# Optimization experiments

Hardware: AMD Instinct MI355X
Metric: run time of the kernel (lower is better)

Reference implementation:

```python
import jax, jax.numpy as jnp
import numpy as np

WL_W = 8   # weight quantization bits (args.wl_weight)
WL_A = 8   # activation quantization bits (args.wl_activate)
EPS = 1e-5


def _quant_ste(x, bits):
    """Symmetric per-tensor uniform quantization with straight-through estimator,
    emulating NeuroSim's wage-style weight/activation quantization in QConv2d."""
    n = float(2 ** (bits - 1) - 1)
    s = jnp.max(jnp.abs(x)) + 1e-12
    xq = jnp.round(x / s * n) / n * s
    return x + jax.lax.stop_gradient(xq - x)


def _qconv(x, w):
    # quantize input and weight, then 3x3 conv, stride 1, padding 1 (NCHW/OIHW)
    xq = _quant_ste(x, WL_A)
    wq = _quant_ste(w, WL_W)
    return jax.lax.conv_general_dilated(
        xq, wq, window_strides=(1, 1), padding=((1, 1), (1, 1)),
        dimension_numbers=('NCHW', 'OIHW', 'NCHW'))


def _bn(x, gamma, beta):
    # training-mode BatchNorm2d: batch statistics over (N, H, W)
    mean = jnp.mean(x, axis=(0, 2, 3), keepdims=True)
    var = jnp.var(x, axis=(0, 2, 3), keepdims=True)
    xn = (x - mean) * jax.lax.rsqrt(var + EPS)
    return xn * gamma[None, :, None, None] + beta[None, :, None, None]


def setup_inputs() -> dict:
    key = jax.random.key(0)
    ks = jax.random.split(key, 3)
    B, C, H, W = 32, 128, 56, 56
    return {
        'x': jax.random.normal(ks[0], (B, C, H, W), dtype=jnp.float32),
        'w1': jax.random.normal(ks[1], (C, C, 3, 3), dtype=jnp.float32) * 0.05,
        'gamma1': jnp.ones((C,), dtype=jnp.float32),
        'beta1': jnp.zeros((C,), dtype=jnp.float32),
        'w2': jax.random.normal(ks[2], (C, C, 3, 3), dtype=jnp.float32) * 0.05,
        'gamma2': jnp.ones((C,), dtype=jnp.float32),
        'beta2': jnp.zeros((C,), dtype=jnp.float32),
    }


def reference(x, w1, gamma1, beta1, w2, gamma2, beta2):
    identity = x  # no downsample
    out = _qconv(x, w1)
    out = _bn(out, gamma1, beta1)
    out = jax.nn.relu(out)
    out = _qconv(out, w2)
    out = _bn(out, gamma2, beta2)
    out = out + identity
    return jax.nn.relu(out)
```

## Files before the change

### kernel.cpp

```cpp
#include <hip/hip_runtime.h>

#define NB 32
#define C 128
#define H 56
#define W 56
#define HWSZ (H*W)
#define ELTS (NB*C*HWSZ)
#define NHW (NB*HWSZ)
#define HP 59
#define SLAB 8192
#define GCONVX 28
#define NBLK (GCONVX*NB)
#define NBLK2 (NBLK*2)
#define PSTRIDE2 (C*NBLK2)

typedef __attribute__((ext_vector_type(8))) short bf16x8;
typedef __attribute__((ext_vector_type(4))) short short4v;
typedef __attribute__((ext_vector_type(4))) float f32x4;
typedef __attribute__((ext_vector_type(4))) int i32x4;

#define SLOT_SX 0
#define SLOT_SW1 1
#define SLOT_SW2 2
#define SLOT_SA2 3
#define SCALE1 8
#define SHIFT1 136
#define SCALE2 264
#define SHIFT2 392

#define META_OFF 0ull
#define META_BYTES 8192ull
#define XQ_OFF 8192ull
#define XQ_BYTES ((unsigned long long)NB*HP*SLAB)
#define A2Q_OFF (XQ_OFF + XQ_BYTES)
#define Y1_OFF (A2Q_OFF + XQ_BYTES)
#define Y_BYTES ((unsigned long long)ELTS*2ull)
#define Y2_OFF (Y1_OFF + Y_BYTES)
#define W1Q_OFF (Y2_OFF + Y_BYTES)
#define WQ_BYTES (9ull*2*128*64)
#define W2Q_OFF (W1Q_OFF + WQ_BYTES)
#define PART_OFF (W2Q_OFF + WQ_BYTES)
#define PART_BYTES (4ull*PSTRIDE2*4ull)

__device__ __forceinline__ short f2bf_rne(float f) {
    unsigned u = __float_as_uint(f);
    return (short)((u + 0x7FFFu + ((u >> 16) & 1u)) >> 16);
}
__device__ __forceinline__ float bf2f(short s) {
    return __uint_as_float(((unsigned)(unsigned short)s) << 16);
}

__global__ void absmax_kernel(const float* __restrict__ p, int n4, unsigned* __restrict__ slot) {
    __shared__ float red[256];
    float m = 0.f;
    int stride = gridDim.x * blockDim.x;
    for (int i = blockIdx.x * blockDim.x + threadIdx.x; i < n4; i += stride) {
        f32x4 v = ((const f32x4*)p)[i];
        m = fmaxf(m, fmaxf(fmaxf(fabsf(v.x), fabsf(v.y)), fmaxf(fabsf(v.z), fabsf(v.w))));
    }
    red[threadIdx.x] = m;
    __syncthreads();
    for (int s = 128; s > 0; s >>= 1) {
        if (threadIdx.x < s) red[threadIdx.x] = fmaxf(red[threadIdx.x], red[threadIdx.x + s]);
        __syncthreads();
    }
    if (threadIdx.x == 0) atomicMax(slot, __float_as_uint(red[0]));
}

__global__ void absmax_w_kernel(const float* __restrict__ w1, const float* __restrict__ w2,
                                unsigned* __restrict__ metau) {
    __shared__ float red[256];
    const float* p = blockIdx.y ? w2 : w1;
    unsigned* slot = metau + (blockIdx.y ? SLOT_SW2 : SLOT_SW1);
    const int n4 = 147456 / 4;
    float m = 0.f;
    int stride = gridDim.x * blockDim.x;
    for (int i = blockIdx.x * blockDim.x + threadIdx.x; i < n4; i += stride) {
        f32x4 v = ((const f32x4*)p)[i];
        m = fmaxf(m, fmaxf(fmaxf(fabsf(v.x), fabsf(v.y)), fmaxf(fabsf(v.z), fabsf(v.w))));
    }
    red[threadIdx.x] = m;
    __syncthreads();
    for (int s = 128; s > 0; s >>= 1) {
        if (threadIdx.x < s) red[threadIdx.x] = fmaxf(red[threadIdx.x], red[threadIdx.x + s]);
        __syncthreads();
    }
    if (threadIdx.x == 0) atomicMax(slot, __float_as_uint(red[0]));
}

__global__ void pad_zero_kernel(char* __restrict__ xq, char* __restrict__ a2q,
                                float* __restrict__ meta) {
    int hp = blockIdx.x;
    int n = blockIdx.y;
    char* base = (blockIdx.z ? a2q : xq) + ((size_t)n * HP + hp) * SLAB;
    int t = threadIdx.x;
    if (blockIdx.z == 0 && blockIdx.x == 0 && blockIdx.y == 0) {
        #pragma unroll
        for (int j = 0; j < 8; ++j) meta[j * 256 + t] = 0.f;
    }
    if (hp == 0 || hp >= 57) {
        f32x4 z = {0.f, 0.f, 0.f, 0.f};
        *(f32x4*)(base + t * 16) = z;
        *(f32x4*)(base + 4096 + t * 16) = z;
    } else {
        if (t < 32) *(int*)(base + t * 4) = 0;
        else        *(int*)(base + 7296 + (t - 32) * 4) = 0;
    }
}

__global__ void quant_w_kernel(const float* __restrict__ w1, const float* __restrict__ w2,
                               const float* __restrict__ meta,
                               char* __restrict__ w1q, char* __restrict__ w2q) {
    const float* w = blockIdx.y ? w2 : w1;
    char* wq = blockIdx.y ? w2q : w1q;
    float qs = 127.f / (meta[blockIdx.y ? SLOT_SW2 : SLOT_SW1] + 1e-12f);
    int idx = blockIdx.x * 256 + threadIdx.x;
    int co = idx >> 7, ci = idx & 127;
    const float* src = w + ((size_t)(co * 128 + ci)) * 9;
    int cc = ci >> 6, cl = ci & 63;
    #pragma unroll
    for (int tap = 0; tap < 9; ++tap) {
        int q = (int)rintf(src[tap] * qs);
        wq[(((size_t)tap * 2 + cc) * 128 + co) * 64 + cl] = (char)q;
    }
}

__global__ void quant_x_kernel(const float* __restrict__ x, const float* __restrict__ meta,
                               char* __restrict__ xq) {
    __shared__ float tile[128][57];
    int h = blockIdx.x, n = blockIdx.y, t = threadIdx.x;
    int ci = t >> 1, seg = (t & 1) * 28;
    const float* row = x + (((size_t)(n * C + ci)) * H + h) * W + seg;
    #pragma unroll
    for (int j = 0; j < 28; j += 4) {
        f32x4 v = *(const f32x4*)(row + j);
        tile[ci][seg + j + 0] = v.x;
        tile[ci][seg + j + 1] = v.y;
        tile[ci][seg + j + 2] = v.z;
        tile[ci][seg + j + 3] = v.w;
    }
    __syncthreads();
    float qs = 127.f / (meta[SLOT_SX] + 1e-12f);
    int w = t & 63, cq = t >> 6;
    if (w < 56) {
        char* slab = xq + ((size_t)n * HP + (h + 1)) * SLAB;
        int wp = w + 1;
        #pragma unroll
        for (int c2 = 0; c2 < 2; ++c2) {
            union { char c[16]; i32x4 v; } u;
            #pragma unroll
            for (int j = 0; j < 16; ++j)
                u.c[j] = (char)(int)rintf(tile[cq * 32 + c2 * 16 + j][w] * qs);
            int L = wp * 128 + cq * 32 + c2 * 16;
            *(i32x4*)(slab + (L ^ ((wp & 7) << 4))) = u.v;
        }
    }
}

__global__ __launch_bounds__(256, 4) void conv_mfma_kernel(
        const char* __restrict__ xq, const char* __restrict__ wq,
        short* __restrict__ y, const float* __restrict__ meta,
        float* __restrict__ part, int slot_in, int slot_w) {
    __shared__ __align__(16) char lds[4 * SLAB + 512];
    const int n = blockIdx.y, h0 = blockIdx.x * 2;
    const int t = threadIdx.x, lane = t & 63;
    const int wv = t >> 6, r = wv >> 1, ch = (wv & 1) * 64;
    const int l15 = lane & 15, lg = lane >> 4;

    const char* slabbase = xq + ((size_t)n * HP + h0) * SLAB;
    #pragma unroll
    for (int s = 0; s < 4; ++s) {
        #pragma unroll
        for (int i = 0; i < 2; ++i) {
            int off = (i * 256 + t) * 16;
            __builtin_amdgcn_global_load_lds(
                (const __attribute__((address_space(1))) unsigned*)(slabbase + s * SLAB + off),
                (__attribute__((address_space(3))) unsigned*)(lds + s * SLAB + off), 16, 0, 0);
        }
    }

    i32x4 acc[4][4] = {};

    #pragma unroll
    for (int kh = 0; kh < 3; ++kh) {
        if (kh == 0)      { asm volatile("s_waitcnt vmcnt(4)" ::: "memory"); }
        else if (kh == 1) { asm volatile("s_waitcnt vmcnt(2)" ::: "memory"); }
        else              { asm volatile("s_waitcnt vmcnt(0)" ::: "memory"); }
        __builtin_amdgcn_s_barrier();
        const char* Bb = lds + (kh + r) * SLAB;
        #pragma unroll
        for (int kw = 0; kw < 3; ++kw) {
            #pragma unroll
            for (int cc = 0; cc < 2; ++cc) {
                const char* wt = wq + (((kh * 3 + kw) * 2 + cc) << 13);
                i32x4 a[4];
                #pragma unroll
                for (int ct = 0; ct < 4; ++ct)
                    a[ct] = *(const i32x4*)(wt + (ch + ct * 16 + l15) * 64 + lg * 16);
                #pragma unroll
                for (int fj = 0; fj < 4; ++fj) {
                    int wpp = fj * 16 + l15 + kw;
                    int L = (wpp << 7) + (cc << 6) + (lg << 4);
                    i32x4 b = *(const i32x4*)(Bb + (L ^ ((wpp & 7) << 4)));
                    #pragma unroll
                    for (int ct = 0; ct < 4; ++ct)
                        acc[ct][fj] = __builtin_amdgcn_mfma_i32_16x16x64_i8(a[ct], b, acc[ct][fj], 0, 0, 0);
                }
            }
        }
    }

    float dq = (meta[slot_in] + 1e-12f) * (meta[slot_w] + 1e-12f) * (1.f / 16129.f);
    short* yrow = y + (((size_t)n * H + (h0 + r)) * W) * C;
    int bcol = (blockIdx.y * GCONVX + blockIdx.x) * 2 + r;

    #pragma unroll
    for (int ct = 0; ct < 4; ++ct) {
        float s1[4] = {}, s2[4] = {}, m1[4], m2[4];
        #pragma unroll
        for (int q = 0; q < 4; ++q) { m1[q] = -1e30f; m2[q] = -1e30f; }
        #pragma unroll
        for (int fj = 0; fj < 4; ++fj) {
            int wo = fj * 16 + l15;
            if (wo < W) {
                short4v pk;
                #pragma unroll
                for (int q = 0; q < 4; ++q) {
                    float v = (float)acc[ct][fj][q] * dq;
                    s1[q] += v;
                    s2[q] += v * v;
                    m1[q] = fmaxf(m1[q], v);
                    m2[q] = fmaxf(m2[q], -v);
                    pk[q] = f2bf_rne(v);
                }
                *(short4v*)(yrow + (size_t)wo * C + ch + ct * 16 + lg * 4) = pk;
            }
        }
        #pragma unroll
        for (int q = 0; q < 4; ++q) {
            #pragma unroll
            for (int m = 1; m < 16; m <<= 1) {
                s1[q] += __shfl_xor(s1[q], m, 64);
                s2[q] += __shfl_xor(s2[q], m, 64);
                m1[q] = fmaxf(m1[q], __shfl_xor(m1[q], m, 64));
                m2[q] = fmaxf(m2[q], __shfl_xor(m2[q], m, 64));
            }
        }
        if (l15 == 0) {
            #pragma unroll
            for (int q = 0; q < 4; ++q) {
                int cch = ch + ct * 16 + lg * 4 + q;
                part[0 * PSTRIDE2 + (size_t)cch * NBLK2 + bcol] = s1[q];
                part[1 * PSTRIDE2 + (size_t)cch * NBLK2 + bcol] = s2[q];
                part[2 * PSTRIDE2 + (size_t)cch * NBLK2 + bcol] = m1[q];
                part[3 * PSTRIDE2 + (size_t)cch * NBLK2 + bcol] = m2[q];
            }
        }
    }
}

__global__ void bn_reduce_kernel(const float* __restrict__ part, float* __restrict__ meta,
                                 const float* __restrict__ gamma, const float* __restrict__ beta,
                                 int scale_off, int shift_off, int amax_slot) {
    __shared__ float r1[256], r2[256], r3[256], r4[256];
    int c = blockIdx.x, t = threadIdx.x;
    const float* ps = part + 0 * PSTRIDE2 + (size_t)c * NBLK2;
    const float* pq = part + 1 * PSTRIDE2 + (size_t)c * NBLK2;
    const float* pm = part + 2 * PSTRIDE2 + (size_t)c * NBLK2;
    const float* pn = part + 3 * PSTRIDE2 + (size_t)c * NBLK2;
    float s1 = 0.f, s2 = 0.f, m1 = -1e30f, m2 = -1e30f;
    for (int i = t; i < NBLK2; i += 256) {
        s1 += ps[i];
        s2 += pq[i];
        m1 = fmaxf(m1, pm[i]);
        m2 = fmaxf(m2, pn[i]);
    }
    r1[t] = s1; r2[t] = s2; r3[t] = m1; r4[t] = m2;
    __syncthreads();
    for (int k = 128; k > 0; k >>= 1) {
        if (t < k) {
            r1[t] += r1[t + k];
            r2[t] += r2[t + k];
            r3[t] = fmaxf(r3[t], r3[t + k]);
            r4[t] = fmaxf(r4[t], r4[t + k]);
        }
        __syncthreads();
    }
    if (t == 0) {
        float mean = r1[0] * (1.f / NHW);
        float var = r2[0] * (1.f / NHW) - mean * mean;
        float istd = rsqrtf(var + 1e-5f);
        float sc = gamma[c] * istd;
        float sh = beta[c] - mean * sc;
        meta[scale_off + c] = sc;
        meta[shift_off + c] = sh;
        if (amax_slot >= 0) {
            float cand = fmaxf(0.f, fmaxf(sc * r3[0] + sh, sc * (-r4[0]) + sh));
            atomicMax((unsigned*)meta + amax_slot, __float_as_uint(cand));
        }
    }
}

__global__ void quant_bnrelu_kernel(const short* __restrict__ y1, const float* __restrict__ meta,
                                    char* __restrict__ a2q) {
    int h = blockIdx.x, n = blockIdx.y, t = threadIdx.x;
    const short* row = y1 + (((size_t)n * H + h) * W) * C;
    float qs = 127.f / (meta[SLOT_SA2] + 1e-12f);
    char* slab = a2q + ((size_t)n * HP + (h + 1)) * SLAB;
    #pragma unroll
    for (int i = 0; i < 2; ++i) {
        int g = i * 256 + t;
        if (g < 448) {
            int w = g >> 3, cg = g & 7;
            bf16x8 v0 = *(const bf16x8*)(row + w * 128 + cg * 16);
            bf16x8 v1 = *(const bf16x8*)(row + w * 128 + cg * 16 + 8);
            union { char c[16]; i32x4 v; } u;
            #pragma unroll
            for (int j = 0; j < 8; ++j) {
                float a = fmaxf(bf2f(v0[j]) * meta[SCALE1 + cg * 16 + j] + meta[SHIFT1 + cg * 16 + j], 0.f);
                u.c[j] = (char)(int)rintf(a * qs);
            }
            #pragma unroll
            for (int j = 0; j < 8; ++j) {
                float a = fmaxf(bf2f(v1[j]) * meta[SCALE1 + cg * 16 + 8 + j] + meta[SHIFT1 + cg * 16 + 8 + j], 0.f);
                u.c[8 + j] = (char)(int)rintf(a * qs);
            }
            int wp = w + 1;
            int L = wp * 128 + cg * 16;
            *(i32x4*)(slab + (L ^ ((wp & 7) << 4))) = u.v;
        }
    }
}

__global__ void final_kernel(const short* __restrict__ y2, const float* __restrict__ x,
                             const float* __restrict__ meta, float* __restrict__ out) {
    __shared__ short tile[56 * 128];
    int h = blockIdx.x, n = blockIdx.y, t = threadIdx.x;
    const short* row = y2 + (((size_t)n * H + h) * W) * C;
    #pragma unroll
    for (int i = 0; i < 4; ++i) {
        int g = i * 256 + t;
        if (g < 896) *(bf16x8*)(tile + g * 8) = *(const bf16x8*)(row + g * 8);
    }
    __syncthreads();
    int c = t >> 1, seg = (t & 1) * 28;
    float sc = meta[SCALE2 + c], sh = meta[SHIFT2 + c];
    const float* xr = x + (((size_t)(n * C + c)) * H + h) * W + seg;
    float* orow = out + (((size_t)(n * C + c)) * H + h) * W + seg;
    #pragma unroll
    for (int j = 0; j < 28; j += 4) {
        f32x4 xv = *(const f32x4*)(xr + j);
        f32x4 o;
        #pragma unroll
        for (int k = 0; k < 4; ++k) {
            float yv = bf2f(tile[(seg + j + k) * 128 + c]);
            o[k] = fmaxf(yv * sc + sh + xv[k], 0.f);
        }
        *(f32x4*)(orow + j) = o;
    }
}

extern "C" void kernel_launch(void* const* d_in, const int* in_sizes, int n_in,
                              void* d_out, int out_size, void* d_ws, size_t ws_size,
                              hipStream_t stream) {
    const float* x      = (const float*)d_in[0];
    const float* w1     = (const float*)d_in[1];
    const float* gamma1 = (const float*)d_in[2];
    const float* beta1  = (const float*)d_in[3];
    const float* w2     = (const float*)d_in[4];
    const float* gamma2 = (const float*)d_in[5];
    const float* beta2  = (const float*)d_in[6];
    float* out = (float*)d_out;
    char* ws = (char*)d_ws;

    float* meta = (float*)(ws + META_OFF);
    unsigned* metau = (unsigned*)meta;
    char* xq   = ws + XQ_OFF;
    char* a2q  = ws + A2Q_OFF;
    short* y1  = (short*)(ws + Y1_OFF);
    short* y2  = (short*)(ws + Y2_OFF);
    char* w1q  = ws + W1Q_OFF;
    char* w2q  = ws + W2Q_OFF;
    float* part = (float*)(ws + PART_OFF);

    pad_zero_kernel<<<dim3(59, 32, 2), 256, 0, stream>>>(xq, a2q, meta);

    absmax_kernel<<<1024, 256, 0, stream>>>(x, ELTS / 4, metau + SLOT_SX);
    absmax_w_kernel<<<dim3(64, 2), 256, 0, stream>>>(w1, w2, metau);
    quant_w_kernel<<<dim3(64, 2), 256, 0, stream>>>(w1, w2, meta, w1q, w2q);

    dim3 ghn(56, 32);
    quant_x_kernel<<<ghn, 256, 0, stream>>>(x, meta, xq);

    dim3 gconv(GCONVX, 32);
    conv_mfma_kernel<<<gconv, 256, 0, stream>>>(xq, w1q, y1, meta, part, SLOT_SX, SLOT_SW1);
    bn_reduce_kernel<<<128, 256, 0, stream>>>(part, meta, gamma1, beta1, SCALE1, SHIFT1, SLOT_SA2);
    quant_bnrelu_kernel<<<ghn, 256, 0, stream>>>(y1, meta, a2q);

    conv_mfma_kernel<<<gconv, 256, 0, stream>>>(a2q, w2q, y2, meta, part, SLOT_SA2, SLOT_SW2);
    bn_reduce_kernel<<<128, 256, 0, stream>>>(part, meta, gamma2, beta2, SCALE2, SHIFT2, -1);

    final_kernel<<<ghn, 256, 0, stream>>>(y2, x, meta, out);
}
```

Baseline: 266.0 us.

## Stage conv output through LDS and restructure BN partial-stat reduction layout

The conv epilogue now writes bf16 results into swizzled LDS and then stores full rows to global memory with 16-byte coalesced writes, instead of scattered 8-byte writes. Per-block BN partial statistics are staged in LDS and written contiguously per block. The BN reduction is split into a 64-block kernel that reduces with atomicAdd and order-preserving atomicMax into meta, plus a small finalize kernel. The aim is to cut uncoalesced global traffic and strided partial reads, at the cost of an extra launch and extra LDS use. It also relies on the meta accumulators being zeroed beforehand, which the shown pad_zero/meta setup must guarantee.

Result: slower. 278.1 us (+4.5%).

```diff
diff --git a/kernel.cpp b/kernel.cpp
--- a/kernel.cpp
+++ b/kernel.cpp
@@ -12,7 +12,6 @@
 #define GCONVX 28
 #define NBLK (GCONVX*NB)
 #define NBLK2 (NBLK*2)
-#define PSTRIDE2 (C*NBLK2)
 
 typedef __attribute__((ext_vector_type(8))) short bf16x8;
 typedef __attribute__((ext_vector_type(4))) short short4v;
@@ -23,10 +22,18 @@
 #define SLOT_SW1 1
 #define SLOT_SW2 2
 #define SLOT_SA2 3
-#define SCALE1 8
-#define SHIFT1 136
-#define SCALE2 264
-#define SHIFT2 392
+#define SUM1 8
+#define SSQ1 136
+#define MAXE1 264
+#define MAXNEG1 392
+#define SCALE1 520
+#define SHIFT1 648
+#define SUM2 776
+#define SSQ2 904
+#define MAXE2 1032
+#define MAXNEG2 1160
+#define SCALE2 1288
+#define SHIFT2 1416
 
 #define META_OFF 0ull
 #define META_BYTES 8192ull
@@ -40,7 +47,7 @@
 #define WQ_BYTES (9ull*2*128*64)
 #define W2Q_OFF (W1Q_OFF + WQ_BYTES)
 #define PART_OFF (W2Q_OFF + WQ_BYTES)
-#define PART_BYTES (4ull*PSTRIDE2*4ull)
+#define PART_BYTES ((unsigned long long)NBLK2*512*4)
 
 __device__ __forceinline__ short f2bf_rne(float f) {
     unsigned u = __float_as_uint(f);
@@ -48,6 +55,14 @@
 }
 __device__ __forceinline__ float bf2f(short s) {
     return __uint_as_float(((unsigned)(unsigned short)s) << 16);
+}
+__device__ __forceinline__ unsigned fenc(float f) {
+    unsigned u = __float_as_uint(f);
+    return (u & 0x80000000u) ? ~u : (u | 0x80000000u);
+}
+__device__ __forceinline__ float fdec(unsigned e) {
+    unsigned u = (e & 0x80000000u) ? (e ^ 0x80000000u) : ~e;
+    return __uint_as_float(u);
 }
 
 __global__ void absmax_kernel(const float* __restrict__ p, int n4, unsigned* __restrict__ slot) {
@@ -211,8 +226,10 @@
     }
 
     float dq = (meta[slot_in] + 1e-12f) * (meta[slot_w] + 1e-12f) * (1.f / 16129.f);
-    short* yrow = y + (((size_t)n * H + (h0 + r)) * W) * C;
-    int bcol = (blockIdx.y * GCONVX + blockIdx.x) * 2 + r;
+
+    __syncthreads();
+    char* ylds = lds;
+    float* slds = (float*)(lds + 28672);
 
     #pragma unroll
     for (int ct = 0; ct < 4; ++ct) {
@@ -233,7 +250,8 @@
                     m2[q] = fmaxf(m2[q], -v);
                     pk[q] = f2bf_rne(v);
                 }
-                *(short4v*)(yrow + (size_t)wo * C + ch + ct * 16 + lg * 4) = pk;
+                int a = r * 14336 + wo * 256 + ch * 2 + ct * 32 + lg * 8;
+                *(short4v*)(ylds + (a ^ ((wo & 7) << 4))) = pk;
             }
         }
         #pragma unroll
@@ -249,55 +267,82 @@
         if (l15 == 0) {
             #pragma unroll
             for (int q = 0; q < 4; ++q) {
-                int cch = ch + ct * 16 + lg * 4 + q;
-                part[0 * PSTRIDE2 + (size_t)cch * NBLK2 + bcol] = s1[q];
-                part[1 * PSTRIDE2 + (size_t)cch * NBLK2 + bcol] = s2[q];
-                part[2 * PSTRIDE2 + (size_t)cch * NBLK2 + bcol] = m1[q];
-                part[3 * PSTRIDE2 + (size_t)cch * NBLK2 + bcol] = m2[q];
-            }
-        }
+                int c = ch + ct * 16 + lg * 4 + q;
+                slds[r * 512 + 0 * 128 + c] = s1[q];
+                slds[r * 512 + 1 * 128 + c] = s2[q];
+                slds[r * 512 + 2 * 128 + c] = m1[q];
+                slds[r * 512 + 3 * 128 + c] = m2[q];
+            }
+        }
+    }
+    __syncthreads();
+
+    short* ybase = y + (((size_t)n * H + h0) * W) * C;
+    #pragma unroll
+    for (int i = 0; i < 7; ++i) {
+        int g = i * 256 + t;
+        int r2 = g >= 896;
+        int rem = g - r2 * 896;
+        int wo = rem >> 4, cb = rem & 15;
+        int a = r2 * 14336 + wo * 256 + cb * 16;
+        bf16x8 v = *(const bf16x8*)(ylds + (a ^ ((wo & 7) << 4)));
+        *(bf16x8*)(ybase + ((size_t)r2 * W + wo) * C + cb * 8) = v;
+    }
+
+    {
+        int bh = t >> 7;
+        int off = t & 127;
+        int p = off >> 5, cs = (off & 31) * 4;
+        f32x4 sv = *(const f32x4*)(slds + bh * 512 + p * 128 + cs);
+        size_t bcol = (size_t)(blockIdx.y * GCONVX + blockIdx.x) * 2 + bh;
+        *(f32x4*)(part + bcol * 512 + p * 128 + cs) = sv;
     }
 }
 
 __global__ void bn_reduce_kernel(const float* __restrict__ part, float* __restrict__ meta,
-                                 const float* __restrict__ gamma, const float* __restrict__ beta,
-                                 int scale_off, int shift_off, int amax_slot) {
-    __shared__ float r1[256], r2[256], r3[256], r4[256];
-    int c = blockIdx.x, t = threadIdx.x;
-    const float* ps = part + 0 * PSTRIDE2 + (size_t)c * NBLK2;
-    const float* pq = part + 1 * PSTRIDE2 + (size_t)c * NBLK2;
-    const float* pm = part + 2 * PSTRIDE2 + (size_t)c * NBLK2;
-    const float* pn = part + 3 * PSTRIDE2 + (size_t)c * NBLK2;
-    float s1 = 0.f, s2 = 0.f, m1 = -1e30f, m2 = -1e30f;
-    for (int i = t; i < NBLK2; i += 256) {
-        s1 += ps[i];
-        s2 += pq[i];
-        m1 = fmaxf(m1, pm[i]);
-        m2 = fmaxf(m2, pn[i]);
-    }
-    r1[t] = s1; r2[t] = s2; r3[t] = m1; r4[t] = m2;
-    __syncthreads();
-    for (int k = 128; k > 0; k >>= 1) {
-        if (t < k) {
-            r1[t] += r1[t + k];
-            r2[t] += r2[t + k];
-            r3[t] = fmaxf(r3[t], r3[t + k]);
-            r4[t] = fmaxf(r4[t], r4[t + k]);
-        }
+                                 int sum_off, int ssq_off, int maxe_off, int maxneg_off) {
+    int t = threadIdx.x, b = blockIdx.x;
+    const float* base = part + (size_t)b * 28 * 512;
+    float vadd = 0.f, vmax = -1e30f;
+    for (int i = 0; i < 28; ++i) {
+        vadd += base[i * 512 + t];
+        vmax = fmaxf(vmax, base[i * 512 + 256 + t]);
+    }
+    int c = t & 127;
+    unsigned* metau = (unsigned*)meta;
+    if (t < 128) {
+        atomicAdd(&meta[sum_off + c], vadd);
+        atomicMax(metau + maxe_off + c, fenc(vmax));
+    } else {
+        atomicAdd(&meta[ssq_off + c], vadd);
+        atomicMax(metau + maxneg_off + c, fenc(vmax));
+    }
+}
+
+__global__ void bn_finalize_kernel(float* __restrict__ meta, int sum_off, int ssq_off,
+                                   int maxe_off, int maxneg_off, int scale_off, int shift_off,
+                                   int amax_slot,
+                                   const float* __restrict__ gamma, const float* __restrict__ beta) {
+    __shared__ float red[128];
+    int c = threadIdx.x;
+    float mean = meta[sum_off + c] * (1.f / NHW);
+    float var = meta[ssq_off + c] * (1.f / NHW) - mean * mean;
+    float istd = rsqrtf(var + 1e-5f);
+    float sc = gamma[c] * istd;
+    float sh = beta[c] - mean * sc;
+    meta[scale_off + c] = sc;
+    meta[shift_off + c] = sh;
+    if (amax_slot >= 0) {
+        float vmax = fdec(((unsigned*)meta)[maxe_off + c]);
+        float vmin = -fdec(((unsigned*)meta)[maxneg_off + c]);
+        float cand = fmaxf(0.f, fmaxf(sc * vmax + sh, sc * vmin + sh));
+        red[c] = cand;
         __syncthreads();
-    }
-    if (t == 0) {
-        float mean = r1[0] * (1.f / NHW);
-        float var = r2[0] * (1.f / NHW) - mean * mean;
-        float istd = rsqrtf(var + 1e-5f);
-        float sc = gamma[c] * istd;
-        float sh = beta[c] - mean * sc;
-        meta[scale_off + c] = sc;
-        meta[shift_off + c] = sh;
-        if (amax_slot >= 0) {
-            float cand = fmaxf(0.f, fmaxf(sc * r3[0] + sh, sc * (-r4[0]) + sh));
-            atomicMax((unsigned*)meta + amax_slot, __float_as_uint(cand));
-        }
+        for (int k = 64; k > 0; k >>= 1) {
+            if (c < k) red[c] = fmaxf(red[c], red[c + k]);
+            __syncthreads();
+        }
+        if (c == 0) meta[amax_slot] = red[0];
     }
 }
 
@@ -394,11 +439,15 @@
 
     dim3 gconv(GCONVX, 32);
     conv_mfma_kernel<<<gconv, 256, 0, stream>>>(xq, w1q, y1, meta, part, SLOT_SX, SLOT_SW1);
-    bn_reduce_kernel<<<128, 256, 0, stream>>>(part, meta, gamma1, beta1, SCALE1, SHIFT1, SLOT_SA2);
+    bn_reduce_kernel<<<64, 256, 0, stream>>>(part, meta, SUM1, SSQ1, MAXE1, MAXNEG1);
+    bn_finalize_kernel<<<1, 128, 0, stream>>>(meta, SUM1, SSQ1, MAXE1, MAXNEG1,
+                                              SCALE1, SHIFT1, SLOT_SA2, gamma1, beta1);
     quant_bnrelu_kernel<<<ghn, 256, 0, stream>>>(y1, meta, a2q);
 
     conv_mfma_kernel<<<gconv, 256, 0, stream>>>(a2q, w2q, y2, meta, part, SLOT_SA2, SLOT_SW2);
-    bn_reduce_kernel<<<128, 256, 0, stream>>>(part, meta, gamma2, beta2, SCALE2, SHIFT2, -1);
+    bn_reduce_kernel<<<64, 256, 0, stream>>>(part, meta, SUM2, SSQ2, MAXE2, MAXNEG2);
+    bn_finalize_kernel<<<1, 128, 0, stream>>>(meta, SUM2, SSQ2, MAXE2, MAXNEG2,
+                                              SCALE2, SHIFT2, -1, gamma2, beta2);
 
     final_kernel<<<ghn, 256, 0, stream>>>(y2, x, meta, out);
 }
```
